# Kernel tuning notes

Hardware: AMD Instinct MI355X
Metric: run time of the kernel (lower is better)

## Reference

```python
import jax, jax.numpy as jnp
import numpy as np

B, C_IN, C_OUT, N, T = 32, 64, 192, 307, 24
DILATIONS = (1, 2)
O3 = C_OUT // 3  # out channels per branch


def setup_inputs() -> dict:
    key = jax.random.key(0)
    ks = iter(jax.random.split(key, 32))
    nrm = lambda shape: 0.05 * jax.random.normal(next(ks), shape, dtype=jnp.float32)
    return {
        "x": jax.random.normal(next(ks), (B, C_IN, N, T), dtype=jnp.float32),
        "adj": jax.random.randint(next(ks), (N, N), 0, 2, dtype=jnp.int32),
        "ln_g": jnp.ones((T,), jnp.float32),
        "ln_b": jnp.zeros((T,), jnp.float32),
        "res_W": nrm((C_OUT, C_IN)), "res_b": nrm((C_OUT,)),
        "ca_W1": nrm((T,)), "ca_W2": nrm((N, T)), "ca_W3": nrm((N,)),
        "cc_W": nrm((O3, C_IN)), "cc_b": nrm((O3,)),
        "ta_W1": nrm((N,)), "ta_W2": nrm((C_IN, N)), "ta_W3": nrm((C_IN,)),
        "tc_W0": nrm((O3, C_IN, 1, 2)), "tc_b0": nrm((O3,)),
        "tc_W1": nrm((O3, O3, 1, 2)), "tc_b1": nrm((O3,)),
        "ga_W1": nrm((T,)), "ga_W2": nrm((C_IN, T)), "ga_W3": nrm((C_IN,)),
        "g_W": nrm((O3, C_IN)),
    }


def layer_norm_lastdim(x, g, b, eps=1e-5):
    mu = jnp.mean(x, axis=-1, keepdims=True)
    var = jnp.var(x, axis=-1, keepdims=True)
    return (x - mu) * jax.lax.rsqrt(var + eps) * g + b


def conv1x1(x, W, b):
    # x: [B,C,N,T], W: [O,C]
    return jnp.einsum("oc,bcnt->bont", W, x) + b[None, :, None, None]


def c_attention(x, W1, W2, W3):
    # channel attention over C; x: [B,C,N,T]
    lhs = jnp.einsum("bcn,nt->bct", jnp.einsum("bcnt,t->bcn", x, W1), W2)  # [B,C,T]
    rhs = jnp.einsum("n,bcnt->bct", W3, x)                                  # [B,C,T]
    att = jax.nn.softmax(jnp.einsum("bct,bdt->bcd", lhs, rhs), axis=-1)     # [B,C,C]
    return jnp.einsum("bcd,bdnt->bcnt", att, x)


def t_attention(x, W1, W2, W3):
    # temporal attention over T; x: [B,C,N,T]
    lhs = jnp.einsum("bct,cn->btn", jnp.einsum("bcnt,n->bct", x, W1), W2)   # [B,T,N]
    rhs = jnp.einsum("c,bcnt->bnt", W3, x)                                   # [B,N,T]
    att = jax.nn.softmax(jnp.einsum("btn,bns->bts", lhs, rhs), axis=-1)      # [B,T,T]
    return jnp.einsum("bts,bcns->bcnt", att, x)


def g_attention(x, adj, W1, W2, W3):
    # graph (spatial) attention over N, masked by adjacency; x: [B,C,N,T]
    lhs = jnp.einsum("bcn,ct->bnt", jnp.einsum("bcnt,t->bcn", x, W1), W2)   # [B,N,T]
    rhs = jnp.einsum("c,bcnt->bnt", W3, x)                                   # [B,N,T]
    scores = jnp.einsum("bnt,bmt->bnm", lhs, rhs)                            # [B,N,N]
    scores = jnp.where(adj[None] > 0, scores, jnp.float32(-1e30))
    att = jax.nn.softmax(scores, axis=-1)
    return jnp.einsum("bnm,bcmt->bcnt", att, x)


def causal_conv(x, W, b, d):
    # Conv2d kernel [1,2], dilation [1,d], pad [0,d] + Chomp(d) == left-pad-only causal conv
    y = jax.lax.conv_general_dilated(
        x, W, window_strides=(1, 1), padding=((0, 0), (d, 0)),
        rhs_dilation=(1, d), dimension_numbers=("NCHW", "OIHW", "NCHW"))
    return y + b[None, :, None, None]


def meam_forward(x, adj, ln_g, ln_b, res_W, res_b, ca_W1, ca_W2, ca_W3, cc_W, cc_b,
                 ta_W1, ta_W2, ta_W3, tc_W0, tc_b0, tc_W1, tc_b1,
                 ga_W1, ga_W2, ga_W3, g_W):
    h = layer_norm_lastdim(x, ln_g, ln_b)
    # CACN branch: channel attention + 1x1 conv
    c_out = conv1x1(c_attention(h, ca_W1, ca_W2, ca_W3), cc_W, cc_b)
    # TACN branch: temporal attention + dilated causal convs
    t_out = t_attention(h, ta_W1, ta_W2, ta_W3)
    t_out = causal_conv(t_out, tc_W0, tc_b0, DILATIONS[0])
    t_out = causal_conv(t_out, tc_W1, tc_b1, DILATIONS[1])
    # GACN branch: graph attention + channel mixing
    g_out = jnp.einsum("oc,bcnt->bont", g_W, g_attention(h, adj, ga_W1, ga_W2, ga_W3))
    out = jnp.concatenate([c_out, t_out, g_out], axis=1)  # [B, C_OUT, N, T]
    return jax.nn.relu(out + conv1x1(x, res_W, res_b))


def reference(x, adj, ln_g, ln_b, res_W, res_b, ca_W1, ca_W2, ca_W3, cc_W, cc_b,
              ta_W1, ta_W2, ta_W3, tc_W0, tc_b0, tc_W1, tc_b1,
              ga_W1, ga_W2, ga_W3, g_W):
    return meam_forward(x, adj, ln_g, ln_b, res_W, res_b, ca_W1, ca_W2, ca_W3, cc_W, cc_b,
                        ta_W1, ta_W2, ta_W3, tc_W0, tc_b0, tc_W1, tc_b1,
                        ga_W1, ga_W2, ga_W3, g_W)
```

## Files before the change

### kernel.cpp

```cpp
#include <hip/hip_runtime.h>
#include <hip/hip_bf16.h>

#define BB 32
#define CC 64
#define NN 307
#define TT 24
#define CO 192
#define NT (NN*TT)
#define GO 1536

using bf16 = __hip_bfloat16;
typedef __attribute__((ext_vector_type(8))) short bf16x8;
typedef __attribute__((ext_vector_type(4))) float f32x4;

#define OFF_ln_g   0
#define OFF_ln_b   24
#define OFF_res_W  48
#define OFF_res_b  12336
#define OFF_ca_W1  12528
#define OFF_ca_W2  12552
#define OFF_ca_W3  19920
#define OFF_cc_W   20227
#define OFF_cc_b   24323
#define OFF_ta_W1  24387
#define OFF_ta_W2  24694
#define OFF_ta_W3  44342
#define OFF_tc_W0  44406
#define OFF_tc_b0  52598
#define OFF_tc_W1  52662
#define OFF_tc_b1  60854
#define OFF_ga_W1  60918
#define OFF_ga_W2  60942
#define OFF_ga_W3  62478
#define OFF_g_W    62542
#define W_TOTAL    66638

__device__ __forceinline__ float xload(const void* p, size_t i, int f) {
  return f ? ((const float*)p)[i] : __bfloat162float(((const bf16*)p)[i]);
}
__device__ __forceinline__ void ostore(void* p, size_t i, float v, int f) {
  if (f) ((float*)p)[i] = v; else ((bf16*)p)[i] = __float2bfloat16(v);
}
__device__ __forceinline__ float oload(const void* p, size_t i, int f) {
  return f ? ((const float*)p)[i] : __bfloat162float(((const bf16*)p)[i]);
}

__global__ void MEAM_44787918963464_kernel() {}

__global__ __launch_bounds__(256) void k_probe(const void* lng_raw, int* flag) {
  if (threadIdx.x == 0 && blockIdx.x == 0) {
    unsigned w = *(const unsigned*)lng_raw;
    *flag = (w == 0x3F800000u) ? 1 : 0;
  }
}

__global__ __launch_bounds__(256) void k_cvt_w(
    const void* p0, const void* p1, const void* p2, const void* p3,
    const void* p4, const void* p5, const void* p6, const void* p7,
    const void* p8, const void* p9, const void* p10, const void* p11,
    const void* p12, const void* p13, const void* p14, const void* p15,
    const void* p16, const void* p17, const void* p18, const void* p19,
    const int* flagp, float* dst) {
  int i = blockIdx.x*256 + threadIdx.x;
  if (i >= W_TOTAL) return;
  const void* ps[20] = {p0,p1,p2,p3,p4,p5,p6,p7,p8,p9,p10,p11,p12,p13,p14,p15,p16,p17,p18,p19};
  const int sz[20] = {24,24,12288,192,24,7368,307,4096,64,307,19648,64,8192,64,8192,64,24,1536,64,4096};
  int f = *flagp;
  int s = 0, base = 0;
  while (i >= base + sz[s]) { base += sz[s]; s++; }
  dst[i] = f ? ((const float*)ps[s])[i-base]
             : __bfloat162float(((const bf16*)ps[s])[i-base]);
}

__global__ __launch_bounds__(256) void k_prep_tc(const float* __restrict__ W,
    bf16* __restrict__ Ag, float* __restrict__ tb_bias) {
  int g = blockIdx.x*256 + threadIdx.x;
  if (g >= CC*CC) return;
  int pI = g >> 6, c = g & 63;
  const float* W0 = W + OFF_tc_W0;
  const float* b0 = W + OFF_tc_b0;
  const float* W1 = W + OFF_tc_W1;
  const float* b1 = W + OFF_tc_b1;
  const float* resW = W + OFF_res_W;
  const float* resb = W + OFF_res_b;
  float m0=0.f,m1=0.f,m2=0.f,m3=0.f, bb0=0.f, bb2=0.f;
  for (int o=0;o<CC;o++){
    float a1v = W1[(pI*CC+o)*2], b1v = W1[(pI*CC+o)*2+1];
    float a0v = W0[(o*CC+c)*2],  b0v = W0[(o*CC+c)*2+1];
    m0 += b1v*b0v; m1 += b1v*a0v; m2 += a1v*b0v; m3 += a1v*a0v;
    bb0 += b1v*b0[o]; bb2 += a1v*b0[o];
  }
  Ag[pI*320 + 0*64 + c] = __float2bfloat16(m0);
  Ag[pI*320 + 1*64 + c] = __float2bfloat16(m1);
  Ag[pI*320 + 2*64 + c] = __float2bfloat16(m2);
  Ag[pI*320 + 3*64 + c] = __float2bfloat16(m3);
  Ag[pI*320 + 4*64 + c] = __float2bfloat16(resW[(64+pI)*CC + c]);
  if (c == 0){
    tb_bias[pI]    = b1[pI] + bb0 + resb[64+pI];
    tb_bias[64+pI] = bb2;
  }
}

__global__ __launch_bounds__(256) void k_prep_A(const float* __restrict__ Mc,
    const float* __restrict__ W, bf16* __restrict__ Apre) {
  int idx = blockIdx.x*256 + threadIdx.x;
  if (idx >= BB*192*128) return;
  int b = idx / 24576;
  int rem = idx - b*24576;
  int p2 = rem >> 7, k = rem & 127;
  const float* resW = W + OFF_res_W;
  const float* gW   = W + OFF_g_W;
  float v;
  if (p2 < 64)       v = (k < 64) ? Mc[b*CC*CC + p2*CC + k] : resW[p2*CC + (k-64)];
  else if (p2 < 128) v = (k < 64) ? gW[(p2-64)*CC + k] : 0.f;
  else               v = (k < 64) ? 0.f : resW[p2*CC + (k-64)];
  Apre[idx] = __float2bfloat16(v);
}

__global__ __launch_bounds__(256) void k_ln(const void* __restrict__ x, const int* flagp,
    const float* __restrict__ W,
    float* __restrict__ mu_o, float* __restrict__ rs_o,
    float* __restrict__ xw1c, float* __restrict__ xw1g) {
  int r = blockIdx.x*256 + threadIdx.x;
  if (r >= BB*CC*NN) return;
  int f = *flagp;
  const float* lng  = W + OFF_ln_g;
  const float* lnb  = W + OFF_ln_b;
  const float* caW1 = W + OFF_ca_W1;
  const float* gaW1 = W + OFF_ga_W1;
  float v[TT];
  if (f) {
    const float4* xp = (const float4*)((const float*)x + (size_t)r*TT);
    #pragma unroll
    for (int i=0;i<6;i++){ float4 q = xp[i]; v[i*4]=q.x; v[i*4+1]=q.y; v[i*4+2]=q.z; v[i*4+3]=q.w; }
  } else {
    const uint4* xp = (const uint4*)((const unsigned short*)x + (size_t)r*TT);
    #pragma unroll
    for (int i=0;i<3;i++){
      uint4 q = xp[i]; unsigned u[4]={q.x,q.y,q.z,q.w};
      #pragma unroll
      for (int k=0;k<4;k++){
        union{unsigned uu;float fl;} lo,hi;
        lo.uu=u[k]<<16; hi.uu=u[k]&0xffff0000u;
        v[i*8+k*2]=lo.fl; v[i*8+k*2+1]=hi.fl;
      }
    }
  }
  float mu = 0.f;
  #pragma unroll
  for (int t=0;t<TT;t++) mu += v[t];
  mu *= (1.f/TT);
  float var = 0.f;
  #pragma unroll
  for (int t=0;t<TT;t++){ float d=v[t]-mu; var += d*d; }
  var *= (1.f/TT);
  float rs = rsqrtf(var + 1e-5f);
  float s1=0.f, s2=0.f;
  #pragma unroll
  for (int t=0;t<TT;t++){
    float hv = (v[t]-mu)*rs*lng[t] + lnb[t];
    s1 += hv*caW1[t];
    s2 += hv*gaW1[t];
  }
  mu_o[r]=mu; rs_o[r]=rs; xw1c[r]=s1; xw1g[r]=s2;
}

__global__ __launch_bounds__(256) void k_prep_ct(const void* __restrict__ x, const int* flagp,
    const float* __restrict__ mu_a, const float* __restrict__ rs_a,
    const float* __restrict__ W, const float* __restrict__ xw1c,
    float* __restrict__ lhsc, float* __restrict__ rhsc, float* __restrict__ xw1t) {
  int i = blockIdx.x*256 + threadIdx.x;
  if (i >= BB*CC*TT) return;
  int f = *flagp;
  const float* lng  = W + OFF_ln_g;
  const float* lnb  = W + OFF_ln_b;
  const float* caW2 = W + OFF_ca_W2;
  const float* caW3 = W + OFF_ca_W3;
  const float* taW1 = W + OFF_ta_W1;
  int t = i % TT; int bc = i / TT;
  float gt = lng[t], bt = lnb[t];
  float l=0.f, rr=0.f, xt=0.f;
  for (int n=0;n<NN;n++){
    int row = bc*NN + n;
    float hv = (xload(x, (size_t)row*TT+t, f) - mu_a[row]) * rs_a[row] * gt + bt;
    l  += xw1c[row]*caW2[n*TT+t];
    rr += caW3[n]*hv;
    xt += taW1[n]*hv;
  }
  lhsc[i]=l; rhsc[i]=rr; xw1t[i]=xt;
}

__global__ __launch_bounds__(256) void k_prep_bn(const void* __restrict__ x, const int* flagp,
    const float* __restrict__ mu_a, const float* __restrict__ rs_a,
    const float* __restrict__ W, const float* __restrict__ xw1g,
    float* __restrict__ rhst, float* __restrict__ rhsg, float* __restrict__ lhsg) {
  int i = blockIdx.x*256 + threadIdx.x;
  if (i >= BB*NN*TT) return;
  int f = *flagp;
  const float* lng  = W + OFF_ln_g;
  const float* lnb  = W + OFF_ln_b;
  const float* taW3 = W + OFF_ta_W3;
  const float* gaW3 = W + OFF_ga_W3;
  const float* gaW2 = W + OFF_ga_W2;
  int t = i % TT; int n = (i/TT)%NN; int b = i/(NN*TT);
  float gt = lng[t], bt = lnb[t];
  float a=0.f,c2=0.f,d=0.f;
  for (int c=0;c<CC;c++){
    int row = (b*CC+c)*NN + n;
    float hv = (xload(x, (size_t)row*TT+t, f) - mu_a[row]) * rs_a[row] * gt + bt;
    a  += taW3[c]*hv;
    c2 += gaW3[c]*hv;
    d  += xw1g[row]*gaW2[c*TT+t];
  }
  rhst[i]=a; rhsg[i]=c2; lhsg[i]=d;
}

__global__ __launch_bounds__(256) void k_lhs_t(const float* __restrict__ xw1t,
    const float* __restrict__ W, float* __restrict__ lhst) {
  int i = blockIdx.x*256 + threadIdx.x;
  if (i >= BB*TT*NN) return;
  const float* taW2 = W + OFF_ta_W2;
  int n = i % NN; int t = (i/NN)%TT; int b = i/(TT*NN);
  float acc=0.f;
  for (int c=0;c<CC;c++)
    acc += xw1t[(b*CC+c)*TT+t]*taW2[c*NN+n];
  lhst[i]=acc;
}

__global__ __launch_bounds__(256) void k_att_c(const float* __restrict__ lhsc,
    const float* __restrict__ rhsc, const float* __restrict__ W,
    float* __restrict__ Mc) {
  int b = blockIdx.x; int tid = threadIdx.x;
  const float* ccW = W + OFF_cc_W;
  __shared__ float lc[CC*TT], rc[CC*TT], sc[CC*(CC+1)];
  for (int e=tid;e<CC*TT;e+=256){
    lc[e]=lhsc[b*CC*TT+e];
    rc[e]=rhsc[b*CC*TT+e];
  }
  __syncthreads();
  for (int e=tid;e<CC*CC;e+=256){
    int c=e>>6, d=e&63; float s=0.f;
    for (int t=0;t<TT;t++) s += lc[c*TT+t]*rc[d*TT+t];
    sc[c*(CC+1)+d]=s;
  }
  __syncthreads();
  if (tid<CC){
    float mx=-1e30f;
    for (int d=0;d<CC;d++) mx=fmaxf(mx, sc[tid*(CC+1)+d]);
    float sum=0.f;
    for (int d=0;d<CC;d++){ float e2=__expf(sc[tid*(CC+1)+d]-mx); sc[tid*(CC+1)+d]=e2; sum+=e2; }
    float inv=1.f/sum;
    for (int d=0;d<CC;d++) sc[tid*(CC+1)+d]*=inv;
  }
  __syncthreads();
  for (int e=tid;e<CC*CC;e+=256){
    int o=e>>6, d=e&63; float acc=0.f;
    for (int c=0;c<CC;c++) acc += ccW[o*CC+c]*sc[c*(CC+1)+d];
    Mc[b*CC*CC+e]=acc;
  }
}

__global__ __launch_bounds__(256) void k_att_t(const float* __restrict__ lhst,
    const float* __restrict__ rhst, float* __restrict__ attt) {
  int b=blockIdx.x, tid=threadIdx.x;
  __shared__ float sc[TT*TT];
  for (int e=tid;e<TT*TT;e+=256){
    int t=e/TT, s=e%TT;
    float acc=0.f;
    for (int n=0;n<NN;n++)
      acc += lhst[(b*TT+t)*NN+n]*rhst[(b*NN+n)*TT+s];
    sc[e]=acc;
  }
  __syncthreads();
  if (tid < TT){
    float mx=-1e30f;
    for (int s=0;s<TT;s++) mx=fmaxf(mx,sc[tid*TT+s]);
    float sum=0.f;
    for (int s=0;s<TT;s++){ float e=__expf(sc[tid*TT+s]-mx); sc[tid*TT+s]=e; sum+=e; }
    float inv=1.f/sum;
    for (int s=0;s<TT;s++) attt[b*TT*TT + tid*TT + s]=sc[tid*TT+s]*inv;
  }
}

__global__ __launch_bounds__(256) void k_scores_g(const float* __restrict__ lhsg,
    const float* __restrict__ rhsg, const int* __restrict__ adj,
    float* __restrict__ Sg) {
  int mt = blockIdx.x, nt = blockIdx.y, b = blockIdx.z;
  int n0 = nt*64, m0 = mt*64, tid = threadIdx.x;
  __shared__ unsigned short Lh[64*40], Ll[64*40], Rh[64*40], Rl[64*40];
  for (int e=tid; e<64*24; e+=256){
    int r=e/24, t=e-(e/24)*24;
    int gn=n0+r, gm=m0+r;
    float lv = (gn<NN)? lhsg[((size_t)b*NN+gn)*TT+t] : 0.f;
    float rv = (gm<NN)? rhsg[((size_t)b*NN+gm)*TT+t] : 0.f;
    bf16 lh=__float2bfloat16(lv); float lhf=__bfloat162float(lh);
    bf16 llo=__float2bfloat16(lv-lhf);
    bf16 rh=__float2bfloat16(rv); float rhf=__bfloat162float(rh);
    bf16 rlo=__float2bfloat16(rv-rhf);
    Lh[r*40+t]=*(unsigned short*)&lh; Ll[r*40+t]=*(unsigned short*)&llo;
    Rh[r*40+t]=*(unsigned short*)&rh; Rl[r*40+t]=*(unsigned short*)&rlo;
  }
  for (int e=tid; e<64*8; e+=256){
    int r=e>>3, t=24+(e&7);
    Lh[r*40+t]=0; Ll[r*40+t]=0; Rh[r*40+t]=0; Rl[r*40+t]=0;
  }
  __syncthreads();
  int lane=tid&63, w=tid>>6, q=lane>>4, lr=lane&15;
  bf16x8 ah = *(const bf16x8*)&Lh[(w*16+lr)*40 + q*8];
  bf16x8 al = *(const bf16x8*)&Ll[(w*16+lr)*40 + q*8];
  f32x4 z4={0.f,0.f,0.f,0.f};
  f32x4 acc[4]={z4,z4,z4,z4};
  #pragma unroll
  for (int ct=0;ct<4;ct++){
    bf16x8 bh = *(const bf16x8*)&Rh[(ct*16+lr)*40 + q*8];
    bf16x8 bl = *(const bf16x8*)&Rl[(ct*16+lr)*40 + q*8];
    acc[ct]=__builtin_amdgcn_mfma_f32_16x16x32_bf16(ah,bh,acc[ct],0,0,0);
    acc[ct]=__builtin_amdgcn_mfma_f32_16x16x32_bf16(ah,bl,acc[ct],0,0,0);
    acc[ct]=__builtin_amdgcn_mfma_f32_16x16x32_bf16(al,bh,acc[ct],0,0,0);
  }
  #pragma unroll
  for (int ct=0;ct<4;ct++){
    int m = m0 + ct*16 + lr;
    #pragma unroll
    for (int r=0;r<4;r++){
      int n = n0 + w*16 + q*4 + r;
      if (n<NN && m<NN){
        float s = acc[ct][r];
        if (adj[n*NN+m] <= 0) s = -1e30f;
        Sg[((size_t)b*NN+n)*NN+m] = s;
      }
    }
  }
}

__global__ __launch_bounds__(256) void k_smax_g(const float* __restrict__ Sg,
    bf16* __restrict__ attgh) {
  int b = blockIdx.y;
  int n = blockIdx.x*4 + (threadIdx.x>>6);
  int lane = threadIdx.x & 63;
  if (n >= NN) return;
  const float* row = Sg + ((size_t)b*NN+n)*NN;
  float v[5]; float mx = -1e30f;
  #pragma unroll
  for (int i=0;i<5;i++){
    int m = lane + i*64;
    v[i] = (m<NN)? row[m] : -1e30f;
    mx = fmaxf(mx, v[i]);
  }
  #pragma unroll
  for (int off=32; off; off>>=1) mx = fmaxf(mx, __shfl_xor(mx, off));
  float sum = 0.f;
  #pragma unroll
  for (int i=0;i<5;i++){
    int m = lane + i*64;
    float e = (m<NN)? __expf(v[i]-mx) : 0.f;
    v[i]=e; sum += e;
  }
  #pragma unroll
  for (int off=32; off; off>>=1) sum += __shfl_xor(sum, off);
  float inv = 1.f/sum;
  bf16* orow = attgh + ((size_t)b*NN+n)*NN;
  #pragma unroll
  for (int i=0;i<5;i++){
    int m = lane + i*64;
    if (m<NN) orow[m] = __float2bfloat16(v[i]*inv);
  }
}

__global__ __launch_bounds__(256) void k_hgc_mfma(
    const void* __restrict__ x, const int* flagp,
    const float* __restrict__ mu_a, const float* __restrict__ rs_a,
    const float* __restrict__ W, const bf16* __restrict__ Apre,
    bf16* __restrict__ hg, bf16* __restrict__ resg, void* __restrict__ out) {
  int jt = blockIdx.x, b = blockIdx.y, tid = threadIdx.x;
  int f = *flagp;
  int j0 = jt*64;
  const float* lng = W + OFF_ln_g;
  const float* lnb = W + OFF_ln_b;
  const float* ccb = W + OFF_cc_b;
  const float* resb= W + OFF_res_b;
  __shared__ unsigned short Bs[64*128];

  {
    int c = tid >> 2, jg = tid & 3;
    float xv[16];
    int jbase = j0 + jg*16;
    size_t xoff = (size_t)(b*CC + c)*NT + jbase;
    if (jbase + 15 < NT) {
      if (f) {
        const float4* xp = (const float4*)((const float*)x + xoff);
        #pragma unroll
        for (int v=0; v<4; v++){ float4 q = xp[v]; xv[v*4]=q.x; xv[v*4+1]=q.y; xv[v*4+2]=q.z; xv[v*4+3]=q.w; }
      } else {
        const uint4* xp = (const uint4*)((const unsigned short*)x + xoff);
        #pragma unroll
        for (int v=0; v<2; v++){
          uint4 q = xp[v]; unsigned u[4]={q.x,q.y,q.z,q.w};
          #pragma unroll
          for (int kk2=0;kk2<4;kk2++){
            union{unsigned uu;float fl;} lo,hi;
            lo.uu=u[kk2]<<16; hi.uu=u[kk2]&0xffff0000u;
            xv[v*8+kk2*2]=lo.fl; xv[v*8+kk2*2+1]=hi.fl;
          }
        }
      }
    } else {
      #pragma unroll
      for (int i=0;i<16;i++){ int j=jbase+i; xv[i] = (j<NT)? xload(x, xoff+i, f) : 0.f; }
    }
    const float* mu_r = mu_a + (b*CC+c)*NN;
    const float* rs_r = rs_a + (b*CC+c)*NN;
    #pragma unroll
    for (int i=0;i<16;i++){
      int j = jbase + i;
      int jl = jg*16 + i;
      float hv = 0.f, xf = 0.f;
      if (j < NT){
        int n = j / 24, t = j - n*24;
        xf = xv[i];
        hv = (xf - mu_r[n]) * rs_r[n] * lng[t] + lnb[t];
      }
      int cs = c ^ ((jl&7)<<3);
      bf16 hb = __float2bfloat16(hv), xb = __float2bfloat16(xf);
      Bs[jl*128 + cs]      = *(unsigned short*)&hb;
      Bs[jl*128 + cs + 64] = *(unsigned short*)&xb;
    }
  }

  int lane = tid & 63, w = tid >> 6;
  int q = lane >> 4, lr = lane & 15;
  bf16x8 afo[4], afh[2], afr[2];
  {
    const unsigned short* Ab = (const unsigned short*)Apre + (size_t)b*24576;
    const unsigned short* r0 = Ab + (w*16 + lr)*128;
    #pragma unroll
    for (int kc=0;kc<4;kc++) afo[kc] = *(const bf16x8*)&r0[kc*32 + q*8];
    const unsigned short* r1 = Ab + (64 + w*16 + lr)*128;
    #pragma unroll
    for (int kc=0;kc<2;kc++) afh[kc] = *(const bf16x8*)&r1[kc*32 + q*8];
    const unsigned short* r2 = Ab + (128 + w*16 + lr)*128;
    #pragma unroll
    for (int kc=0;kc<2;kc++) afr[kc] = *(const bf16x8*)&r2[(kc+2)*32 + q*8];
  }
  f32x4 z4 = {0.f,0.f,0.f,0.f};
  f32x4 acco[4] = {z4,z4,z4,z4};
  f32x4 acch[4] = {z4,z4,z4,z4};
  f32x4 accr[4] = {z4,z4,z4,z4};
  __syncthreads();

  #pragma unroll
  for (int ct=0; ct<4; ct++){
    int jl = ct*16 + lr;
    int sw = ((jl&7)<<3);
    #pragma unroll
    for (int kc=0; kc<4; kc++){
      int ke = (kc*32 + q*8) ^ sw;
      bf16x8 bfr = *(const bf16x8*)&Bs[jl*128 + ke];
      acco[ct] = __builtin_amdgcn_mfma_f32_16x16x32_bf16(afo[kc], bfr, acco[ct], 0,0,0);
      if (kc < 2)
        acch[ct] = __builtin_amdgcn_mfma_f32_16x16x32_bf16(afh[kc], bfr, acch[ct], 0,0,0);
      else
        accr[ct] = __builtin_amdgcn_mfma_f32_16x16x32_bf16(afr[kc-2], bfr, accr[ct], 0,0,0);
    }
  }

  #pragma unroll
  for (int ct=0;ct<4;ct++){
    int jl = ct*16 + lr;
    int j = j0 + jl;
    if (j < NT){
      #pragma unroll
      for (int r=0;r<4;r++){
        int p2 = w*16 + q*4 + r;
        float v = acco[ct][r] + ccb[p2] + resb[p2];
        ostore(out, ((size_t)b*CO + p2)*NT + j, fmaxf(v,0.f), f);
      }
      int n = j/24, t2 = j - n*24;
      size_t hb2 = ((size_t)b*NN + n)*GO + t2;
      #pragma unroll
      for (int r=0;r<4;r++){
        int o = w*16 + q*4 + r;
        hg[hb2 + o*TT] = __float2bfloat16(acch[ct][r]);
      }
      #pragma unroll
      for (int r=0;r<4;r++){
        int p3 = w*16 + q*4 + r;
        resg[((size_t)b*CC + p3)*NT + j] = __float2bfloat16(accr[ct][r] + resb[128+p3]);
      }
    }
  }
}

__global__ __launch_bounds__(256) void k_gemm_g(const bf16* __restrict__ attgh,
    const bf16* __restrict__ hg, const bf16* __restrict__ resg,
    const int* flagp, void* __restrict__ out) {
  int jt = blockIdx.x, nt = blockIdx.y, b = blockIdx.z;
  int tid = threadIdx.x;
  int f = *flagp;
  int n0 = nt*64, j0 = jt*64;
  __shared__ unsigned short As[64*72];
  __shared__ unsigned short Bs[64*72];
  int lane = tid & 63, w = tid >> 6;
  int q = lane >> 4, lr = lane & 15;
  f32x4 z4 = {0.f,0.f,0.f,0.f};
  f32x4 acc[4] = {z4,z4,z4,z4};
  const unsigned short* Ag = (const unsigned short*)attgh + (size_t)b*NN*NN;
  const unsigned short* Bg = (const unsigned short*)hg + (size_t)b*NN*GO;
  for (int m0=0;m0<NN;m0+=64){
    for (int u=tid; u<512; u+=256){
      int r=u>>3, kb=(u&7)*8;
      int gn=n0+r, gm=m0+kb;
      if (gn<NN && gm+7<NN){
        *(uint4*)&As[r*72+kb] = *(const uint4*)&Ag[(size_t)gn*NN + gm];
      } else {
        for (int i2=0;i2<8;i2++){
          int m=gm+i2;
          As[r*72+kb+i2] = (gn<NN && m<NN) ? Ag[(size_t)gn*NN+m] : 0;
        }
      }
    }
    for (int u=tid; u<512; u+=256){
      int m = u>>3, jb = (u&7)*8;
      int gm = m0 + m;
      unsigned short s[8];
      if (gm < NN){
        *(uint4*)s = *(const uint4*)&Bg[(size_t)gm*GO + j0 + jb];
      } else {
        #pragma unroll
        for (int i2=0;i2<8;i2++) s[i2]=0;
      }
      int mb = m>>3, ml2 = m&7;
      #pragma unroll
      for (int i2=0;i2<8;i2++){
        int j = jb + i2;
        int col = ((mb ^ (j>>3)) << 3) | ml2;
        Bs[j*72 + col] = s[i2];
      }
    }
    __syncthreads();
    #pragma unroll
    for (int kk=0;kk<64;kk+=32){
      bf16x8 af = *(const bf16x8*)&As[(w*16+lr)*72 + kk + q*8];
      #pragma unroll
      for (int ct=0;ct<4;ct++){
        int jrow = ct*16+lr;
        int kb = kk + q*8;
        int col = (((kb>>3) ^ (jrow>>3)) << 3);
        bf16x8 bfr = *(const bf16x8*)&Bs[jrow*72 + col];
        acc[ct] = __builtin_amdgcn_mfma_f32_16x16x32_bf16(af, bfr, acc[ct], 0,0,0);
      }
    }
    __syncthreads();
  }
  #pragma unroll
  for (int ct=0;ct<4;ct++){
    #pragma unroll
    for (int r=0;r<4;r++){
      int n = n0 + w*16 + q*4 + r;
      if (n >= NN) continue;
      int j = j0 + ct*16 + lr;
      int o = j/TT, t2 = j%TT;
      size_t idx = ((size_t)b*CO + 128 + o)*NT + (size_t)n*TT + t2;
      float v = acc[ct][r] + __bfloat162float(resg[((size_t)b*CC + o)*NT + (size_t)n*TT + t2]);
      ostore(out, idx, fmaxf(v, 0.f), f);
    }
  }
}

__global__ __launch_bounds__(256) void k_cmix(const float* __restrict__ Mc,
    const void* __restrict__ x, const int* flagp,
    const float* __restrict__ mu_a, const float* __restrict__ rs_a,
    const float* __restrict__ W, void* __restrict__ out) {
  int jt=blockIdx.x, b=blockIdx.y, tid=threadIdx.x;
  int f = *flagp;
  int j0=jt*64;
  const float* lng = W + OFF_ln_g;
  const float* lnb = W + OFF_ln_b;
  const float* ccb = W + OFF_cc_b;
  __shared__ float Ms[CC*64];
  __shared__ float Hs[CC*64];
  for (int e=tid;e<CC*64;e+=256){
    int o=e&63, d=e>>6;
    Ms[e]=Mc[b*CC*CC + o*CC + d];
  }
  for (int e=tid;e<CC*64;e+=256){
    int d=e>>6, j=e&63; int jj=j0+j;
    float hv = 0.f;
    if (jj<NT){
      int n = jj/TT, t = jj%TT;
      int row = (b*CC+d)*NN + n;
      hv = (xload(x, (size_t)(b*CC+d)*NT + jj, f) - mu_a[row]) * rs_a[row] * lng[t] + lnb[t];
    }
    Hs[e]=hv;
  }
  __syncthreads();
  int ti=tid&15, tj=tid>>4;
  float acc[4][4]={};
  for (int d=0;d<CC;d++){
    float4 a4=*(const float4*)&Ms[d*64+ti*4];
    float4 b4=*(const float4*)&Hs[d*64+tj*4];
    float av[4]={a4.x,a4.y,a4.z,a4.w};
    float bv[4]={b4.x,b4.y,b4.z,b4.w};
    for (int i=0;i<4;i++)
      for (int j=0;j<4;j++) acc[i][j]+=av[i]*bv[j];
  }
  for (int i=0;i<4;i++){
    int o=ti*4+i; float bias=ccb[o];
    for (int j=0;j<4;j++){
      int jj=j0+tj*4+j;
      if (jj<NT)
        ostore(out, ((size_t)b*CO+o)*NT+jj, acc[i][j]+bias, f);
    }
  }
}

__global__ __launch_bounds__(256) void k_graph(const float* __restrict__ lhsg,
    const float* __restrict__ rhsg, const int* __restrict__ adj,
    const void* __restrict__ x, const int* flagp,
    const float* __restrict__ mu_a, const float* __restrict__ rs_a,
    const float* __restrict__ W, void* __restrict__ out) {
  int n = blockIdx.x, b = blockIdx.y, tid = threadIdx.x;
  int f = *flagp;
  const float* lng = W + OFF_ln_g;
  const float* lnb = W + OFF_ln_b;
  const float* gW  = W + OFF_g_W;
  __shared__ float ls[TT];
  __shared__ float sv[NN];
  __shared__ float red[256];
  __shared__ float wl[NN];
  __shared__ int   ml[NN];
  __shared__ int   cnt;
  __shared__ float z[CC*TT];
  __shared__ float Gs[CC*CC];
  __shared__ float gs[TT], bs[TT];
  if (tid < TT){
    ls[tid] = lhsg[(b*NN+n)*TT + tid];
    gs[tid] = lng[tid]; bs[tid] = lnb[tid];
  }
  for (int e=tid;e<CC*CC;e+=256) Gs[e]=gW[e];
  __syncthreads();
  float lmax = -1e30f;
  for (int m=tid;m<NN;m+=256){
    float s = -1e30f;
    if (adj[n*NN+m] > 0){
      const float* rr = rhsg + ((size_t)b*NN+m)*TT;
      float acc=0.f;
      for (int t=0;t<TT;t++) acc += ls[t]*rr[t];
      s = acc;
    }
    sv[m]=s; lmax=fmaxf(lmax,s);
  }
  red[tid]=lmax; __syncthreads();
  for (int k=128;k>0;k>>=1){ if (tid<k) red[tid]=fmaxf(red[tid],red[tid+k]); __syncthreads(); }
  float mx = red[0]; __syncthreads();
  float lsum=0.f;
  for (int m=tid;m<NN;m+=256){
    float e = (sv[m] > -1e29f) ? __expf(sv[m]-mx) : 0.f;
    sv[m]=e; lsum+=e;
  }
  red[tid]=lsum; __syncthreads();
  for (int k=128;k>0;k>>=1){ if (tid<k) red[tid]+=red[tid+k]; __syncthreads(); }
  float inv = 1.f/red[0];
  if (tid==0){
    int c=0;
    for (int m=0;m<NN;m++) if (sv[m]!=0.f){ ml[c]=m; wl[c]=sv[m]*inv; c++; }
    cnt=c;
  }
  __syncthreads();
  int K = cnt;
  {
    int c = tid>>2, tg = tid&3;
    float acc[6]={0,0,0,0,0,0};
    float s0 = 0.f;
    const float* mu_r = mu_a + (b*CC+c)*NN;
    const float* rs_r = rs_a + (b*CC+c)*NN;
    size_t xbase = (size_t)(b*CC+c)*NT;
    for (int k=0;k<K;k++){
      int m = ml[k];
      float wr = wl[k]*rs_r[m];
      s0 += wr*mu_r[m];
      size_t xm = xbase + m*TT + tg*6;
      for (int j=0;j<6;j++) acc[j] += wr*xload(x, xm+j, f);
    }
    for (int j=0;j<6;j++){
      int t = tg*6+j;
      z[c*TT+t] = gs[t]*(acc[j]-s0) + bs[t];
    }
  }
  __syncthreads();
  {
    int o = tid>>2, tg = tid&3;
    float acc[6]={0,0,0,0,0,0};
    for (int c=0;c<CC;c++){
      float gwv = Gs[o*CC+c];
      const float* zr = &z[c*TT + tg*6];
      for (int j=0;j<6;j++) acc[j] += gwv*zr[j];
    }
    size_t base = ((size_t)b*CO + 128 + o)*NT + n*TT + tg*6;
    for (int j=0;j<6;j++)
      ostore(out, base+j, acc[j], f);
  }
}

__global__ __launch_bounds__(256) void k_tbranch(const void* __restrict__ x, const int* flagp,
    const float* __restrict__ mu_a, const float* __restrict__ rs_a,
    const float* __restrict__ W, const float* __restrict__ attt,
    void* __restrict__ out, int fuse) {
  int chunk = blockIdx.x, b = blockIdx.y, tid = threadIdx.x;
  int f = *flagp;
  int n0 = chunk*4;
  const float* lng = W + OFF_ln_g;
  const float* lnb = W + OFF_ln_b;
  const float* W0  = W + OFF_tc_W0;
  const float* b0  = W + OFF_tc_b0;
  const float* W1  = W + OFF_tc_W1;
  const float* b1  = W + OFF_tc_b1;
  __shared__ float hs[256*25];
  __shared__ float at[TT*TT];
  for (int e=tid;e<CC*4*TT;e+=256){
    int c=e/(4*TT), rem=e%(4*TT), i=rem/TT, t=rem%TT;
    int n=n0+i;
    float hv=0.f;
    if (n<NN){
      int row=(b*CC+c)*NN+n;
      hv = (xload(x,(size_t)row*TT+t,f) - mu_a[row]) * rs_a[row] * lng[t] + lnb[t];
    }
    hs[(c*4+i)*25+t] = hv;
  }
  for (int e=tid;e<TT*TT;e+=256) at[e]=attt[b*TT*TT+e];
  __syncthreads();
  {
    float r[TT], o2[TT];
    float* myrow = &hs[tid*25];
    #pragma unroll
    for (int s=0;s<TT;s++) r[s]=myrow[s];
    for (int t=0;t<TT;t++){
      float a=0.f;
      #pragma unroll
      for (int s=0;s<TT;s++) a += at[t*TT+s]*r[s];
      o2[t]=a;
    }
    #pragma unroll
    for (int t=0;t<TT;t++) myrow[t]=o2[t];
  }
  __syncthreads();
  {
    int o = tid>>2, i = tid&3;
    float acc[TT];
    float bb = b0[o];
    for (int t=0;t<TT;t++) acc[t]=bb;
    for (int c=0;c<CC;c++){
      float wa = W0[(o*CC+c)*2], wb = W0[(o*CC+c)*2+1];
      const float* row = &hs[(c*4+i)*25];
      acc[0] += wb*row[0];
      #pragma unroll
      for (int t=1;t<TT;t++) acc[t] += wa*row[t-1] + wb*row[t];
    }
    __syncthreads();
    float* myrow = &hs[tid*25];
    #pragma unroll
    for (int t=0;t<TT;t++) myrow[t]=acc[t];
  }
  __syncthreads();
  {
    int o2 = tid>>2, i = tid&3;
    int n = n0+i;
    float acc[TT];
    float bb = b1[o2];
    for (int t=0;t<TT;t++) acc[t]=bb;
    for (int o=0;o<CC;o++){
      float wa = W1[(o2*CC+o)*2], wb = W1[(o2*CC+o)*2+1];
      const float* row = &hs[(o*4+i)*25];
      acc[0] += wb*row[0];
      acc[1] += wb*row[1];
      #pragma unroll
      for (int t=2;t<TT;t++) acc[t] += wa*row[t-2] + wb*row[t];
    }
    if (n<NN){
      size_t base = (((size_t)b*CO + 64 + o2)*NN + n)*TT;
      if (fuse){
        for (int t=0;t<TT;t++){
          float v = acc[t] + oload(out, base+t, f);
          ostore(out, base+t, fmaxf(v,0.f), f);
        }
      } else {
        for (int t=0;t<TT;t++) ostore(out, base+t, acc[t], f);
      }
    }
  }
}

__device__ __forceinline__ void tb_load_raw(const void* __restrict__ x, int f, int b, int c, int nn,
    float* h) {
  if (nn < NN) {
    size_t off = (size_t)(b*CC + c)*NT + (size_t)nn*TT;
    if (f) {
      const float4* xp = (const float4*)((const float*)x + off);
      #pragma unroll
      for (int v=0; v<6; v++){
        float4 q = xp[v];
        h[v*4+0]=q.x; h[v*4+1]=q.y; h[v*4+2]=q.z; h[v*4+3]=q.w;
      }
    } else {
      const uint4* xp = (const uint4*)((const unsigned short*)x + off);
      #pragma unroll
      for (int v=0; v<3; v++){
        uint4 q = xp[v];
        unsigned wsv[4] = {q.x,q.y,q.z,q.w};
        #pragma unroll
        for (int k=0;k<4;k++){
          union { unsigned u; float fl; } lo, hi;
          lo.u = wsv[k] << 16; hi.u = wsv[k] & 0xffff0000u;
          h[v*8 + k*2] = lo.fl; h[v*8 + k*2 + 1] = hi.fl;
        }
      }
    }
  } else {
    #pragma unroll
    for (int t=0;t<TT;t++) h[t]=0.f;
  }
}

__global__ __launch_bounds__(256) void k_tb_mfma(
    const void* __restrict__ x, const int* flagp,
    const float* __restrict__ mu_a, const float* __restrict__ rs_a,
    const float* __restrict__ W, const float* __restrict__ attt,
    const bf16* __restrict__ Agm, const float* __restrict__ tb_bias,
    void* __restrict__ out) {
  int chunk = blockIdx.x, b = blockIdx.y, tid = threadIdx.x;
  int f = *flagp;
  int n0 = chunk*8;
  const float* lng = W + OFF_ln_g;
  const float* lnb = W + OFF_ln_b;
  __shared__ unsigned short Bs[8*27*64];
  __shared__ unsigned short Xs[8*24*64];

  for (int e=tid; e<8*3*64; e+=256){
    int n = e/192, rem = e%192, s = rem>>6, cz = rem&63;
    Bs[((n*27+s)<<6) + cz] = 0;
  }

  int c  = tid & 63;
  int nA = tid >> 6;
  float h0[TT], h1[TT];
  tb_load_raw(x, f, b, c, n0+nA,   h0);
  tb_load_raw(x, f, b, c, n0+nA+4, h1);
  #pragma unroll
  for (int t=0;t<TT;t++){
    int cs = c ^ ((t&7)<<3);
    bf16 v0 = __float2bfloat16(h0[t]);
    bf16 v1 = __float2bfloat16(h1[t]);
    Xs[(nA*24+t)*64 + cs]     = *reinterpret_cast<unsigned short*>(&v0);
    Xs[((nA+4)*24+t)*64 + cs] = *reinterpret_cast<unsigned short*>(&v1);
  }
  {
    int nn0 = n0+nA, nn1 = n0+nA+4;
    if (nn0 < NN){
      int r = (b*CC+c)*NN + nn0; float mu = mu_a[r], rs = rs_a[r];
      #pragma unroll
      for (int t=0;t<TT;t++) h0[t] = (h0[t]-mu)*rs*lng[t] + lnb[t];
    }
    if (nn1 < NN){
      int r = (b*CC+c)*NN + nn1; float mu = mu_a[r], rs = rs_a[r];
      #pragma unroll
      for (int t=0;t<TT;t++) h1[t] = (h1[t]-mu)*rs*lng[t] + lnb[t];
    }
  }
  const float* att_b = attt + b*TT*TT;
  for (int t=0;t<TT;t++){
    float a0=0.f, a1=0.f;
    #pragma unroll
    for (int s=0;s<TT;s++){
      float wv = att_b[t*TT+s];
      a0 += wv*h0[s]; a1 += wv*h1[s];
    }
    int sI = t+3;
    int cs = c ^ ((sI&7)<<3);
    bf16 v0 = __float2bfloat16(a0);
    bf16 v1 = __float2bfloat16(a1);
    Bs[((nA*27+sI)<<6) + cs]     = *reinterpret_cast<unsigned short*>(&v0);
    Bs[(((nA+4)*27+sI)<<6) + cs] = *reinterpret_cast<unsigned short*>(&v1);
  }

  int lane = tid & 63, w = tid >> 6;
  int q = lane >> 4, lr = lane & 15;
  bf16x8 af[10];
  const unsigned short* Arow = (const unsigned short*)Agm + (size_t)(w*16+lr)*320;
  #pragma unroll
  for (int kc=0;kc<10;kc++)
    af[kc] = *(const bf16x8*)&Arow[kc*32 + q*8];

  f32x4 z4 = {0.f,0.f,0.f,0.f};
  f32x4 acc[12] = {z4,z4,z4,z4,z4,z4,z4,z4,z4,z4,z4,z4};
  __syncthreads();

  #pragma unroll
  for (int ct=0; ct<12; ct++){
    int col = ct*16 + lr;
    int nl = col/24, t = col - nl*24;
    #pragma unroll
    for (int kc=0;kc<8;kc++){
      int tap = kc>>1;
      int s = t + 3 - tap;
      int cb = ((kc&1)*32 + q*8) ^ ((s&7)<<3);
      bf16x8 bfr = *(const bf16x8*)&Bs[((nl*27+s)<<6) + cb];
      acc[ct] = __builtin_amdgcn_mfma_f32_16x16x32_bf16(af[kc], bfr, acc[ct], 0,0,0);
    }
    #pragma unroll
    for (int kc2=0;kc2<2;kc2++){
      int cb = (kc2*32 + q*8) ^ ((t&7)<<3);
      bf16x8 bfr = *(const bf16x8*)&Xs[(nl*24+t)*64 + cb];
      acc[ct] = __builtin_amdgcn_mfma_f32_16x16x32_bf16(af[8+kc2], bfr, acc[ct], 0,0,0);
    }
  }

  #pragma unroll
  for (int ct=0;ct<12;ct++){
    int col = ct*16 + lr;
    int nl = col/24, t = col - nl*24;
    int nn = n0 + nl;
    if (nn < NN){
      #pragma unroll
      for (int r=0;r<4;r++){
        int pI = w*16 + q*4 + r;
        size_t idx = ((size_t)b*CO + 64 + pI)*NT + (size_t)nn*TT + t;
        float v = acc[ct][r] + tb_bias[pI] + (t>=2 ? tb_bias[64+pI] : 0.f);
        ostore(out, idx, fmaxf(v, 0.f), f);
      }
    }
  }
}

__global__ __launch_bounds__(256) void k_res_final(const void* __restrict__ x, const int* flagp,
    const float* __restrict__ W, void* __restrict__ out) {
  int jt=blockIdx.x, ot=blockIdx.y, b=blockIdx.z; int tid=threadIdx.x;
  int f = *flagp;
  int j0=jt*64, o0=ot*64;
  const float* resW = W + OFF_res_W;
  const float* resb = W + OFF_res_b;
  __shared__ float Ws[CC*64];
  __shared__ float Xs[CC*64];
  for (int e=tid;e<CC*64;e+=256){
    int o=e&63, c=e>>6;
    Ws[e] = resW[(o0+o)*CC + c];
  }
  for (int e=tid;e<CC*64;e+=256){
    int c=e>>6, j=e&63; int jj=j0+j;
    Xs[e] = (jj<NT) ? xload(x, (size_t)(b*CC+c)*NT + jj, f) : 0.f;
  }
  __syncthreads();
  int ti=tid&15, tj=tid>>4;
  float acc[4][4]={};
  for (int k=0;k<CC;k++){
    float4 a4=*(const float4*)&Ws[k*64+ti*4];
    float4 b4=*(const float4*)&Xs[k*64+tj*4];
    float av[4]={a4.x,a4.y,a4.z,a4.w};
    float bv[4]={b4.x,b4.y,b4.z,b4.w};
    for (int i=0;i<4;i++)
      for (int j=0;j<4;j++) acc[i][j]+=av[i]*bv[j];
  }
  for (int i=0;i<4;i++){
    int o=o0+ti*4+i; float bias=resb[o];
    for (int j=0;j<4;j++){
      int jj=j0+tj*4+j;
      if (jj<NT){
        size_t idx=((size_t)b*CO+o)*NT+jj;
        float v = acc[i][j] + bias + oload(out, idx, f);
        ostore(out, idx, fmaxf(v,0.f), f);
      }
    }
  }
}

extern "C" void kernel_launch(void* const* d_in, const int* in_sizes, int n_in,
                              void* d_out, int out_size, void* d_ws, size_t ws_size,
                              hipStream_t stream) {
  const void* x     = d_in[0];
  const int*  adj   = (const int*)d_in[1];
  void* out = d_out;

  float* p = (float*)d_ws;
  int*   flagp = (int*)p; p += 4;
  float* Wf  = p; p += W_TOTAL;
  float* mu_a = p; p += (size_t)BB*CC*NN;
  float* rs_a = p; p += (size_t)BB*CC*NN;
  float* xw1c = p; p += (size_t)BB*CC*NN;
  float* xw1g = p; p += (size_t)BB*CC*NN;
  float* xw1t = p; p += (size_t)BB*CC*TT;
  float* lhsc = p; p += (size_t)BB*CC*TT;
  float* rhsc = p; p += (size_t)BB*CC*TT;
  float* rhst = p; p += (size_t)BB*NN*TT;
  float* rhsg = p; p += (size_t)BB*NN*TT;
  float* lhsg = p; p += (size_t)BB*NN*TT;
  float* lhst = p; p += (size_t)BB*TT*NN;
  float* attt = p; p += (size_t)BB*TT*TT;
  float* Mc   = p; p += (size_t)BB*CC*CC;
  bf16*  Agm  = (bf16*)p; p += 10240;
  float* tb_bias = p; p += 128;
  bf16*  Apre = (bf16*)p; p += (size_t)BB*192*128/2;
  float* Sg   = p; p += (size_t)BB*NN*NN + 16;
  bf16*  attgh = (bf16*)p; p += (size_t)BB*NN*NN/2 + 16;
  bf16*  resg = (bf16*)p; p += (size_t)BB*CC*NT/2 + 16;
  bf16*  hg   = (bf16*)p;
  size_t need = ((char*)(hg + (size_t)BB*NN*GO)) - (char*)d_ws;
  bool gemm_path = (ws_size >= need);

  k_probe<<<dim3(1), dim3(256), 0, stream>>>(d_in[2], flagp);
  k_cvt_w<<<dim3((W_TOTAL+255)/256), dim3(256), 0, stream>>>(
      d_in[2], d_in[3], d_in[4], d_in[5], d_in[6], d_in[7], d_in[8], d_in[9],
      d_in[10], d_in[11], d_in[12], d_in[13], d_in[14], d_in[15], d_in[16],
      d_in[17], d_in[18], d_in[19], d_in[20], d_in[21], flagp, Wf);
  k_ln<<<dim3((BB*CC*NN+255)/256), dim3(256), 0, stream>>>(x, flagp, Wf, mu_a, rs_a, xw1c, xw1g);
  k_prep_ct<<<dim3((BB*CC*TT+255)/256), dim3(256), 0, stream>>>(x, flagp, mu_a, rs_a, Wf, xw1c, lhsc, rhsc, xw1t);
  k_prep_bn<<<dim3((BB*NN*TT+255)/256), dim3(256), 0, stream>>>(x, flagp, mu_a, rs_a, Wf, xw1g, rhst, rhsg, lhsg);
  k_lhs_t<<<dim3((BB*TT*NN+255)/256), dim3(256), 0, stream>>>(xw1t, Wf, lhst);
  k_att_c<<<dim3(BB), dim3(256), 0, stream>>>(lhsc, rhsc, Wf, Mc);
  k_att_t<<<dim3(BB), dim3(256), 0, stream>>>(lhst, rhst, attt);
  if (gemm_path) {
    k_prep_tc<<<dim3(16), dim3(256), 0, stream>>>(Wf, Agm, tb_bias);
    k_prep_A<<<dim3((BB*192*128+255)/256), dim3(256), 0, stream>>>(Mc, Wf, Apre);
    int ntile = (NN+63)/64;
    k_scores_g<<<dim3(ntile, ntile, BB), dim3(256), 0, stream>>>(lhsg, rhsg, adj, Sg);
    k_smax_g<<<dim3((NN+3)/4, BB), dim3(256), 0, stream>>>(Sg, attgh);
    k_hgc_mfma<<<dim3((NT+63)/64, BB), dim3(256), 0, stream>>>(x, flagp, mu_a, rs_a, Wf, Apre, hg, resg, out);
    k_tb_mfma<<<dim3((NN+7)/8, BB), dim3(256), 0, stream>>>(x, flagp, mu_a, rs_a, Wf, attt, Agm, tb_bias, out);
    k_gemm_g<<<dim3(GO/64, (NN+63)/64, BB), dim3(256), 0, stream>>>(attgh, hg, resg, flagp, out);
  } else {
    k_cmix<<<dim3((NT+63)/64, BB), dim3(256), 0, stream>>>(Mc, x, flagp, mu_a, rs_a, Wf, out);
    k_graph<<<dim3(NN, BB), dim3(256), 0, stream>>>(lhsg, rhsg, adj, x, flagp, mu_a, rs_a, Wf, out);
    k_tbranch<<<dim3((NN+3)/4, BB), dim3(256), 0, stream>>>(x, flagp, mu_a, rs_a, Wf, attt, out, 0);
    k_res_final<<<dim3((NT+63)/64, 3, BB), dim3(256), 0, stream>>>(x, flagp, Wf, out);
  }
}
```

Measured before the change: 755.0 us.

## Fuse layer-norm stats and channel/temporal reductions into one per-(b,c) kernel

Merges the per-row layer-norm kernel and the per-(b,c,t) reduction over N into a single kernel with one block per (b,c). The block stages the whole 307x24 slice in shared memory, computes the row statistics, then reduces over N using 10 thread groups and a shared-memory tree. This removes one launch and a second strided global read of x plus the statistics arrays, and it replaces the old prep_ct pattern of 2048 threads each looping over N with uncoalesced loads. The cost is about 30KB of LDS per block, which limits occupancy, and part of each block idles during the group reduction.

```diff
diff --git a/kernel.cpp b/kernel.cpp
--- a/kernel.cpp
+++ b/kernel.cpp
@@ -117,77 +117,91 @@
   Apre[idx] = __float2bfloat16(v);
 }
 
-__global__ __launch_bounds__(256) void k_ln(const void* __restrict__ x, const int* flagp,
+__global__ __launch_bounds__(256) void k_lnct(const void* __restrict__ x, const int* flagp,
     const float* __restrict__ W,
-    float* __restrict__ mu_o, float* __restrict__ rs_o,
-    float* __restrict__ xw1c, float* __restrict__ xw1g) {
-  int r = blockIdx.x*256 + threadIdx.x;
-  if (r >= BB*CC*NN) return;
+    float* __restrict__ mu_a, float* __restrict__ rs_a,
+    float* __restrict__ xw1c, float* __restrict__ xw1g,
+    float* __restrict__ lhsc, float* __restrict__ rhsc, float* __restrict__ xw1t) {
+  int bc = blockIdx.x;
+  int tid = threadIdx.x;
   int f = *flagp;
   const float* lng  = W + OFF_ln_g;
   const float* lnb  = W + OFF_ln_b;
   const float* caW1 = W + OFF_ca_W1;
   const float* gaW1 = W + OFF_ga_W1;
-  float v[TT];
+  const float* caW2 = W + OFF_ca_W2;
+  const float* caW3 = W + OFF_ca_W3;
+  const float* taW1 = W + OFF_ta_W1;
+  __shared__ float xs[NN*25];
+  __shared__ float mus[NN], rss[NN], w1c[NN];
+  __shared__ float red[3*240];
+  size_t base = (size_t)bc * NT;
   if (f) {
-    const float4* xp = (const float4*)((const float*)x + (size_t)r*TT);
-    #pragma unroll
-    for (int i=0;i<6;i++){ float4 q = xp[i]; v[i*4]=q.x; v[i*4+1]=q.y; v[i*4+2]=q.z; v[i*4+3]=q.w; }
+    const float4* xp = (const float4*)((const float*)x + base);
+    for (int e=tid; e<NT/4; e+=256){
+      float4 q = xp[e];
+      int n = e/6; int t0 = e*4 - n*24;
+      float* d = &xs[n*25 + t0];
+      d[0]=q.x; d[1]=q.y; d[2]=q.z; d[3]=q.w;
+    }
   } else {
-    const uint4* xp = (const uint4*)((const unsigned short*)x + (size_t)r*TT);
-    #pragma unroll
-    for (int i=0;i<3;i++){
-      uint4 q = xp[i]; unsigned u[4]={q.x,q.y,q.z,q.w};
+    const uint4* xp = (const uint4*)((const unsigned short*)x + base);
+    for (int e=tid; e<NT/8; e+=256){
+      uint4 q = xp[e]; unsigned u[4]={q.x,q.y,q.z,q.w};
+      int n = e/3; int t0 = e*8 - n*24;
+      float* d = &xs[n*25 + t0];
       #pragma unroll
       for (int k=0;k<4;k++){
         union{unsigned uu;float fl;} lo,hi;
         lo.uu=u[k]<<16; hi.uu=u[k]&0xffff0000u;
-        v[i*8+k*2]=lo.fl; v[i*8+k*2+1]=hi.fl;
-      }
-    }
-  }
-  float mu = 0.f;
-  #pragma unroll
-  for (int t=0;t<TT;t++) mu += v[t];
-  mu *= (1.f/TT);
-  float var = 0.f;
-  #pragma unroll
-  for (int t=0;t<TT;t++){ float d=v[t]-mu; var += d*d; }
-  var *= (1.f/TT);
-  float rs = rsqrtf(var + 1e-5f);
-  float s1=0.f, s2=0.f;
-  #pragma unroll
-  for (int t=0;t<TT;t++){
-    float hv = (v[t]-mu)*rs*lng[t] + lnb[t];
-    s1 += hv*caW1[t];
-    s2 += hv*gaW1[t];
-  }
-  mu_o[r]=mu; rs_o[r]=rs; xw1c[r]=s1; xw1g[r]=s2;
-}
-
-__global__ __launch_bounds__(256) void k_prep_ct(const void* __restrict__ x, const int* flagp,
-    const float* __restrict__ mu_a, const float* __restrict__ rs_a,
-    const float* __restrict__ W, const float* __restrict__ xw1c,
-    float* __restrict__ lhsc, float* __restrict__ rhsc, float* __restrict__ xw1t) {
-  int i = blockIdx.x*256 + threadIdx.x;
-  if (i >= BB*CC*TT) return;
-  int f = *flagp;
-  const float* lng  = W + OFF_ln_g;
-  const float* lnb  = W + OFF_ln_b;
-  const float* caW2 = W + OFF_ca_W2;
-  const float* caW3 = W + OFF_ca_W3;
-  const float* taW1 = W + OFF_ta_W1;
-  int t = i % TT; int bc = i / TT;
-  float gt = lng[t], bt = lnb[t];
-  float l=0.f, rr=0.f, xt=0.f;
-  for (int n=0;n<NN;n++){
-    int row = bc*NN + n;
-    float hv = (xload(x, (size_t)row*TT+t, f) - mu_a[row]) * rs_a[row] * gt + bt;
-    l  += xw1c[row]*caW2[n*TT+t];
-    rr += caW3[n]*hv;
-    xt += taW1[n]*hv;
-  }
-  lhsc[i]=l; rhsc[i]=rr; xw1t[i]=xt;
+        d[k*2]=lo.fl; d[k*2+1]=hi.fl;
+      }
+    }
+  }
+  __syncthreads();
+  for (int n=tid; n<NN; n+=256){
+    const float* row = &xs[n*25];
+    float mu=0.f;
+    #pragma unroll
+    for (int t=0;t<TT;t++) mu += row[t];
+    mu *= (1.f/TT);
+    float var=0.f;
+    #pragma unroll
+    for (int t=0;t<TT;t++){ float d=row[t]-mu; var += d*d; }
+    var *= (1.f/TT);
+    float rs = rsqrtf(var+1e-5f);
+    float s1=0.f, s2=0.f;
+    #pragma unroll
+    for (int t=0;t<TT;t++){
+      float hv=(row[t]-mu)*rs*lng[t]+lnb[t];
+      s1+=hv*caW1[t]; s2+=hv*gaW1[t];
+    }
+    mus[n]=mu; rss[n]=rs; w1c[n]=s1;
+    int gi = bc*NN+n;
+    mu_a[gi]=mu; rs_a[gi]=rs; xw1c[gi]=s1; xw1g[gi]=s2;
+  }
+  __syncthreads();
+  int t = tid % TT, g = tid / TT;
+  if (g < 10){
+    float gt=lng[t], bt=lnb[t];
+    float l=0.f, rr=0.f, xt=0.f;
+    for (int n=g; n<NN; n+=10){
+      float hv=(xs[n*25+t]-mus[n])*rss[n]*gt+bt;
+      l += w1c[n]*caW2[n*TT+t];
+      rr+= caW3[n]*hv;
+      xt+= taW1[n]*hv;
+    }
+    red[g*TT+t]=l; red[240+g*TT+t]=rr; red[480+g*TT+t]=xt;
+  }
+  __syncthreads();
+  if (tid < TT){
+    float L=0.f,R=0.f,X=0.f;
+    #pragma unroll
+    for (int g2=0; g2<10; g2++){
+      L+=red[g2*TT+tid]; R+=red[240+g2*TT+tid]; X+=red[480+g2*TT+tid];
+    }
+    lhsc[bc*TT+tid]=L; rhsc[bc*TT+tid]=R; xw1t[bc*TT+tid]=X;
+  }
 }
 
 __global__ __launch_bounds__(256) void k_prep_bn(const void* __restrict__ x, const int* flagp,
@@ -1010,8 +1024,7 @@
       d_in[2], d_in[3], d_in[4], d_in[5], d_in[6], d_in[7], d_in[8], d_in[9],
       d_in[10], d_in[11], d_in[12], d_in[13], d_in[14], d_in[15], d_in[16],
       d_in[17], d_in[18], d_in[19], d_in[20], d_in[21], flagp, Wf);
-  k_ln<<<dim3((BB*CC*NN+255)/256), dim3(256), 0, stream>>>(x, flagp, Wf, mu_a, rs_a, xw1c, xw1g);
-  k_prep_ct<<<dim3((BB*CC*TT+255)/256), dim3(256), 0, stream>>>(x, flagp, mu_a, rs_a, Wf, xw1c, lhsc, rhsc, xw1t);
+  k_lnct<<<dim3(BB*CC), dim3(256), 0, stream>>>(x, flagp, Wf, mu_a, rs_a, xw1c, xw1g, lhsc, rhsc, xw1t);
   k_prep_bn<<<dim3((BB*NN*TT+255)/256), dim3(256), 0, stream>>>(x, flagp, mu_a, rs_a, Wf, xw1g, rhst, rhsg, lhsg);
   k_lhs_t<<<dim3((BB*TT*NN+255)/256), dim3(256), 0, stream>>>(xw1t, Wf, lhst);
   k_att_c<<<dim3(BB), dim3(256), 0, stream>>>(lhsc, rhsc, Wf, Mc);
```

Measured after the change: 659.9 us. 1.14x faster.
